# Optimization experiments

Measured on AMD Instinct MI355X. Metric: run time of the kernel, lower is better.

Reference implementation:

```python
import jax, jax.numpy as jnp
import numpy as np

B, S, I = 64, 32, 64
N_ITEMS = 100000
E, H = 256, 128


def setup_inputs() -> dict:
    key = jax.random.key(0)
    k_len, k_ids, k_ut, k_emb, k_wih, k_whh, k_a1, k_a2, k_vt = jax.random.split(key, 9)
    n_sess = B * S
    # ragged session lengths in [2, I] -> trailing zero padding, all sessions valid
    lengths = jax.random.randint(k_len, (n_sess,), 2, I + 1)
    ids = jax.random.randint(k_ids, (n_sess, I), 1, N_ITEMS + 1)
    pad_mask = jnp.arange(I)[None, :] < lengths[:, None]
    item_id = (ids * pad_mask).reshape(B, S, I).astype(jnp.int32)
    eval_from = jnp.zeros((B,), dtype=jnp.int32)
    u_type = jax.random.randint(k_ut, (B,), 0, 5).astype(jnp.int32)
    sc = 0.05
    emb = jax.random.normal(k_emb, (N_ITEMS + 1, E), jnp.float32) * sc
    emb = emb.at[0].set(0.0)  # padding_idx=0
    W_ih = jax.random.normal(k_wih, (3 * H, E), jnp.float32) * sc
    W_hh = jax.random.normal(k_whh, (3 * H, H), jnp.float32) * sc
    b_ih = jnp.zeros((3 * H,), jnp.float32)
    b_hh = jnp.zeros((3 * H,), jnp.float32)
    W_a1 = jax.random.normal(k_a1, (H, H), jnp.float32) * sc
    W_a2 = jax.random.normal(k_a2, (H, H), jnp.float32) * sc
    W_vt = jax.random.normal(k_vt, (1, H), jnp.float32) * sc
    return {"item_id": item_id, "eval_from": eval_from, "u_type": u_type,
            "emb": emb, "W_ih": W_ih, "W_hh": W_hh, "b_ih": b_ih, "b_hh": b_hh,
            "W_a1": W_a1, "W_a2": W_a2, "W_vt": W_vt}


def _gru(x, lengths, W_ih, W_hh, b_ih, b_hh):
    # x: [L, N, E]; packed-GRU semantics: state frozen past each length,
    # outputs zero at padded steps (matches pad_packed_sequence).
    L, N, _ = x.shape
    Hh = W_hh.shape[1]

    def step(h, inp):
        xt, t = inp
        gi = xt @ W_ih.T + b_ih           # [N, 3H]
        gh = h @ W_hh.T + b_hh
        i_r, i_z, i_n = jnp.split(gi, 3, axis=-1)
        h_r, h_z, h_n = jnp.split(gh, 3, axis=-1)
        r = jax.nn.sigmoid(i_r + h_r)
        z = jax.nn.sigmoid(i_z + h_z)
        n = jnp.tanh(i_n + r * h_n)
        h_new = (1.0 - z) * n + z * h
        valid = (t < lengths)[:, None]
        h_next = jnp.where(valid, h_new, h)
        out = jnp.where(valid, h_new, 0.0)
        return h_next, out

    h0 = jnp.zeros((N, Hh), x.dtype)
    hT, outs = jax.lax.scan(step, h0, (x, jnp.arange(L)))
    return outs, hT  # outs: [L, N, H], hT: [N, H]


def reference(item_id, eval_from, u_type, emb, W_ih, W_hh, b_ih, b_hh, W_a1, W_a2, W_vt):
    b, s, i = item_id.shape
    ids = jnp.clip(item_id, 0)
    allow = jnp.arange(s)[None, :] >= eval_from[:, None]        # [B, S]
    ids = ids * allow[:, :, None].astype(ids.dtype)
    sess = ids.reshape(b * s, i)                                # [N, I]
    lengths = (sess != 0).sum(1)                                # all >= 2 by construction
    n = sess.shape[0]
    target = sess[jnp.arange(n), lengths - 1]
    len_in = lengths - 1
    L = i - 1  # static L_in_max; extra padded steps are masked out
    mask = (jnp.arange(L)[None, :] < len_in[:, None])           # [N, L]
    inp = sess[:, :L] * mask.astype(sess.dtype)
    x = emb[inp]                                                # [N, L, E] (dropout=identity, eval)
    outs, ht = _gru(x.transpose(1, 0, 2), len_in, W_ih, W_hh, b_ih, b_hh)
    gru = outs.transpose(1, 0, 2)                               # [N, L, H]
    q1 = jnp.einsum('nlh,kh->nlk', gru, W_a1)
    q2 = (ht @ W_a2.T)[:, None, :]
    alpha = jnp.einsum('nlh,oh->nlo', jax.nn.sigmoid(q1 + q2), W_vt)[..., 0] * mask
    c_loc = jnp.einsum('nl,nlh->nh', alpha, gru)
    reps = jnp.concatenate([c_loc, ht], axis=1)                 # [N, 2H] (ct dropout=identity)
    u = jnp.repeat(u_type, s)
    return reps, target, u
```

## Files before the change

### kernel.cpp

```cpp
#include <hip/hip_runtime.h>
#include <hip/hip_bf16.h>

#define NSESS 2048
#define NI 64
#define LL 63
#define EE 256
#define HH 128
#define GG 384

typedef __attribute__((ext_vector_type(8))) short short8;
typedef __attribute__((ext_vector_type(4))) float f32x4;

static __device__ __forceinline__ unsigned short f2b(float f) {
  union { float f; unsigned u; } v; v.f = f;
  unsigned r = (v.u + 0x7FFFu + ((v.u >> 16) & 1u)) >> 16;
  return (unsigned short)r;
}
static __device__ __forceinline__ float b2f(unsigned short s) {
  union { unsigned u; float f; } v; v.u = ((unsigned)s) << 16;
  return v.f;
}
static __device__ __forceinline__ float lo16(unsigned u) {
  union { unsigned v; float f; } x; x.v = u << 16; return x.f;
}
static __device__ __forceinline__ float hi16(unsigned u) {
  union { unsigned v; float f; } x; x.v = u & 0xFFFF0000u; return x.f;
}
static __device__ __forceinline__ float sigmoidf_(float x) {
  return 1.f / (1.f + __expf(-x));
}
static __device__ __forceinline__ float tanh2_(float y) {
  float e = __expf(2.f * y);
  return 1.f - 2.f / (1.f + e);
}
static __device__ __forceinline__ void barrier_lds_only() {
  asm volatile("s_waitcnt lgkmcnt(0)" ::: "memory");
  __builtin_amdgcn_sched_barrier(0);
  __builtin_amdgcn_s_barrier();
  __builtin_amdgcn_sched_barrier(0);
}

__global__ __launch_bounds__(64) void prep_kernel(const int* __restrict__ item_id,
                                                  const int* __restrict__ eval_from,
                                                  const int* __restrict__ u_type,
                                                  int* __restrict__ len_in,
                                                  int* __restrict__ inp,
                                                  float* __restrict__ out) {
  int n = blockIdx.x;
  int lane = threadIdx.x;
  int b = n >> 5, s = n & 31;
  int allow = (s >= eval_from[b]) ? 1 : 0;
  int id = item_id[n * NI + lane];
  if (id < 0) id = 0;
  id *= allow;
  unsigned long long m = __ballot(id != 0);
  int length = __popcll(m);
  int li = length - 1;
  int tv = __shfl(id, (length > 0) ? (length - 1) : 0, 64);
  int target = (length > 0) ? tv : 0;
  if (lane < LL) inp[n * LL + lane] = (lane < li) ? id : 0;
  if (lane == 0) {
    len_in[n] = li;
    out[NSESS * 256 + n] = (float)target;
    out[NSESS * 256 + NSESS + n] = (float)u_type[b];
  }
}

__global__ __launch_bounds__(256) void cvt_weights(const float* __restrict__ W_ih,
                                                   const float* __restrict__ W_hh,
                                                   const float* __restrict__ W_a1,
                                                   unsigned short* __restrict__ Wb,
                                                   unsigned short* __restrict__ Whs,
                                                   unsigned short* __restrict__ Wa1b) {
  int i = blockIdx.x * 256 + threadIdx.x;
  Wb[i] = f2b(W_ih[i]);
  if (i < GG * HH) Whs[i] = f2b(W_hh[i]);
  if (i < HH * HH) Wa1b[i] = f2b(W_a1[i]);
}

__global__ __launch_bounds__(512, 2) void gemm_in(const float* __restrict__ emb,
                                                  const unsigned short* __restrict__ Wb,
                                                  const float* __restrict__ b_ih,
                                                  const int* __restrict__ inp,
                                                  unsigned short* __restrict__ gi) {
  constexpr int XP = 264;
  __shared__ unsigned short Ash[2][16 * XP];

  const int t = threadIdx.x;
  const int lane = t & 63, w = t >> 6;
  const int ccol = lane & 15, kg = lane >> 4;
  const int g0 = w * 48;

  short8 bfr[3][8];
#pragma unroll
  for (int nt = 0; nt < 3; ++nt) {
    const unsigned short* wrow = Wb + (long)(g0 + nt * 16 + ccol) * EE + kg * 8;
#pragma unroll
    for (int c = 0; c < 8; ++c) bfr[nt][c] = *(const short8*)(wrow + c * 32);
  }
  float bias[3];
#pragma unroll
  for (int nt = 0; nt < 3; ++nt) bias[nt] = b_ih[g0 + nt * 16 + ccol];

  const int tile0 = blockIdx.x * 8;
  const int srow = t >> 5;
  const int scol = (t & 31) * 8;

  {
    long rid = inp[tile0 * 16 + srow];
    const float* x = emb + rid * EE + scol;
    float4 a0 = *(const float4*)x, a1 = *(const float4*)(x + 4);
    short8 v;
    v[0]=(short)f2b(a0.x); v[1]=(short)f2b(a0.y); v[2]=(short)f2b(a0.z); v[3]=(short)f2b(a0.w);
    v[4]=(short)f2b(a1.x); v[5]=(short)f2b(a1.y); v[6]=(short)f2b(a1.z); v[7]=(short)f2b(a1.w);
    *(short8*)(&Ash[0][srow * XP + scol]) = v;
  }
  __syncthreads();

  for (int i = 0; i < 8; ++i) {
    const int cur = i & 1;
    const int m0 = (tile0 + i) * 16;

    float4 a0, a1;
    if (i + 1 < 8) {
      long rid = inp[(tile0 + i + 1) * 16 + srow];
      const float* x = emb + rid * EE + scol;
      a0 = *(const float4*)x; a1 = *(const float4*)(x + 4);
    }

    f32x4 acc[3];
#pragma unroll
    for (int nt = 0; nt < 3; ++nt)
      acc[nt] = (f32x4){bias[nt], bias[nt], bias[nt], bias[nt]};
#pragma unroll
    for (int c = 0; c < 8; ++c) {
      short8 af = *(const short8*)(&Ash[cur][ccol * XP + c * 32 + kg * 8]);
#pragma unroll
      for (int nt = 0; nt < 3; ++nt)
        acc[nt] = __builtin_amdgcn_mfma_f32_16x16x32_bf16(af, bfr[nt][c], acc[nt], 0, 0, 0);
    }

    long base[4];
#pragma unroll
    for (int j = 0; j < 4; ++j) {
      int m = m0 + kg * 4 + j;
      int n = m / 63;
      int l = m - 63 * n;
      base[j] = ((long)l * NSESS + n) * GG;
    }
#pragma unroll
    for (int nt = 0; nt < 3; ++nt) {
      int g = g0 + nt * 16 + ccol;
#pragma unroll
      for (int j = 0; j < 4; ++j)
        gi[base[j] + g] = f2b(acc[nt][j]);
    }

    if (i + 1 < 8) {
      short8 v;
      v[0]=(short)f2b(a0.x); v[1]=(short)f2b(a0.y); v[2]=(short)f2b(a0.z); v[3]=(short)f2b(a0.w);
      v[4]=(short)f2b(a1.x); v[5]=(short)f2b(a1.y); v[6]=(short)f2b(a1.z); v[7]=(short)f2b(a1.w);
      *(short8*)(&Ash[cur ^ 1][srow * XP + scol]) = v;
    }
    barrier_lds_only();
  }
}

__global__ __launch_bounds__(512) void gru_mfma(const unsigned short* __restrict__ Whs,
                                                const float* __restrict__ b_hh,
                                                const unsigned short* __restrict__ gi,
                                                const int* __restrict__ len_in,
                                                unsigned short* __restrict__ outs,
                                                float* __restrict__ ht,
                                                float* __restrict__ out) {
  __shared__ unsigned short ring[2 * 2048];

  const int t = threadIdx.x;
  const int w = t >> 6, lane = t & 63;
  const int ccol = lane & 15, kg = lane >> 4;
  const int n0 = blockIdx.x * 16;
  const int jh = w * 16 + ccol;
  const int p0 = w * 16 + kg * 4;
  const int swz = (ccol & 7) << 3;

  short8 bfr[3][4];
#pragma unroll
  for (int cls = 0; cls < 3; ++cls) {
    const unsigned short* wrow = Whs + (long)(cls * HH + jh) * HH;
#pragma unroll
    for (int c = 0; c < 4; ++c)
      bfr[cls][c] = *(const short8*)(wrow + c * 32 + kg * 8);
  }
  f32x4 bhv[3];
#pragma unroll
  for (int cls = 0; cls < 3; ++cls)
    bhv[cls] = *(const f32x4*)(b_hh + cls * HH + p0);

  const int li = len_in[n0 + ccol];
  float hold[4] = {0.f, 0.f, 0.f, 0.f};

  for (int idx = t; idx < 2 * 2048; idx += 512) ring[idx] = 0;

  const unsigned short* gbase = gi + (long)(n0 + ccol) * GG + p0;
  const long lstride = (long)NSESS * GG;
#define GA(l, cls) ((const uint2*)(gbase + (long)(l) * lstride + (cls) * HH))

  uint2 gA[3], gB[3];
#pragma unroll
  for (int cls = 0; cls < 3; ++cls) gA[cls] = *GA(0, cls);
#pragma unroll
  for (int cls = 0; cls < 3; ++cls) gB[cls] = *GA(1, cls);

  barrier_lds_only();

  auto step = [&](int l, uint2 (&gbuf)[3]) {
    float gvv[3][4];
#pragma unroll
    for (int cls = 0; cls < 3; ++cls) {
      gvv[cls][0] = lo16(gbuf[cls].x); gvv[cls][1] = hi16(gbuf[cls].x);
      gvv[cls][2] = lo16(gbuf[cls].y); gvv[cls][3] = hi16(gbuf[cls].y);
    }
    if (l + 2 < LL) {
#pragma unroll
      for (int cls = 0; cls < 3; ++cls) gbuf[cls] = *GA(l + 2, cls);
    }

    const unsigned short* rb = ring + ((l + 1) & 1) * 2048 + ccol * HH;
    short8 hf[4];
#pragma unroll
    for (int c = 0; c < 4; ++c)
      hf[c] = *(const short8*)(rb + ((c * 32 + kg * 8) ^ swz));

    f32x4 acc[3];
#pragma unroll
    for (int cls = 0; cls < 3; ++cls) {
      acc[cls] = bhv[cls];
#pragma unroll
      for (int c = 0; c < 4; ++c)
        acc[cls] = __builtin_amdgcn_mfma_f32_16x16x32_bf16(bfr[cls][c], hf[c], acc[cls], 0, 0, 0);
    }

    bool valid = (l < li);
#pragma unroll
    for (int j = 0; j < 4; ++j) {
      float rg = sigmoidf_(gvv[0][j] + acc[0][j]);
      float zg = sigmoidf_(gvv[1][j] + acc[1][j]);
      float ng = tanh2_(gvv[2][j] + rg * acc[2][j]);
      float hnew = ng + zg * (hold[j] - ng);
      hold[j] = valid ? hnew : hold[j];
    }
    uint2 hp;
    hp.x = (unsigned)f2b(hold[0]) | ((unsigned)f2b(hold[1]) << 16);
    hp.y = (unsigned)f2b(hold[2]) | ((unsigned)f2b(hold[3]) << 16);
    *(uint2*)(ring + (l & 1) * 2048 + ccol * HH + (((w * 16 + kg * 4)) ^ swz)) = hp;
    uint2 ov = valid ? hp : (uint2){0u, 0u};
    *(uint2*)(outs + ((long)(n0 + ccol) * LL + l) * HH + p0) = ov;
    barrier_lds_only();
  };

  for (int b2 = 0; b2 < 31; ++b2) {
    step(2 * b2, gA);
    step(2 * b2 + 1, gB);
  }
  step(62, gA);
#undef GA

  f32x4 hv = {hold[0], hold[1], hold[2], hold[3]};
  *(f32x4*)(ht + (long)(n0 + ccol) * HH + p0) = hv;
  *(f32x4*)(out + (long)(n0 + ccol) * 256 + HH + p0) = hv;
}

__global__ __launch_bounds__(256) void attn(const unsigned short* __restrict__ outs,
                                            const float* __restrict__ ht,
                                            const unsigned short* __restrict__ Wa1b,
                                            const float* __restrict__ W_a2,
                                            const float* __restrict__ W_vt,
                                            const int* __restrict__ len_in,
                                            float* __restrict__ out) {
  constexpr int OP = HH + 8;
  __shared__ unsigned short o_l[64 * OP];
  __shared__ float q2s[HH];
  __shared__ float wvt[HH];
  __shared__ float hts[HH];
  __shared__ float aw[4][64];
  __shared__ float alphas[64];

  const int n = blockIdx.x;
  const int t = threadIdx.x;
  const int lane = t & 63, wv = t >> 6;
  const int ccol = lane & 15, kg = lane >> 4;
  const int li = len_in[n];

  const unsigned* src = (const unsigned*)(outs + (long)n * LL * HH);
  for (int idx = t; idx < LL * 64; idx += 256) {
    int r = idx >> 6, c2 = idx & 63;
    ((unsigned*)(o_l + r * OP))[c2] = src[r * 64 + c2];
  }
  if (t < 64) ((unsigned*)(o_l + 63 * OP))[t] = 0;
  if (t < HH) { hts[t] = ht[(long)n * HH + t]; wvt[t] = W_vt[t]; }

  short8 bfr[2][4];
#pragma unroll
  for (int nt = 0; nt < 2; ++nt) {
    int G = wv * 32 + nt * 16 + ccol;
#pragma unroll
    for (int c = 0; c < 4; ++c)
      bfr[nt][c] = *(const short8*)(Wa1b + (long)G * HH + c * 32 + kg * 8);
  }
  __syncthreads();

  if (t < HH) {
    float a = 0.f;
    const float* w2 = W_a2 + t * HH;
    for (int k = 0; k < HH; ++k) a += hts[k] * w2[k];
    q2s[t] = a;
  }
  __syncthreads();

  f32x4 acc[4][2];
#pragma unroll
  for (int mt = 0; mt < 4; ++mt)
#pragma unroll
    for (int nt = 0; nt < 2; ++nt) acc[mt][nt] = (f32x4){0.f, 0.f, 0.f, 0.f};
#pragma unroll
  for (int mt = 0; mt < 4; ++mt) {
#pragma unroll
    for (int c = 0; c < 4; ++c) {
      short8 af = *(const short8*)(o_l + (mt * 16 + ccol) * OP + c * 32 + kg * 8);
#pragma unroll
      for (int nt = 0; nt < 2; ++nt)
        acc[mt][nt] = __builtin_amdgcn_mfma_f32_16x16x32_bf16(af, bfr[nt][c], acc[mt][nt], 0, 0, 0);
    }
  }

  float q2v[2], wvv[2];
#pragma unroll
  for (int nt = 0; nt < 2; ++nt) {
    int cg = wv * 32 + nt * 16 + ccol;
    q2v[nt] = q2s[cg]; wvv[nt] = wvt[cg];
  }
#pragma unroll
  for (int mt = 0; mt < 4; ++mt) {
    float part[4] = {0.f, 0.f, 0.f, 0.f};
#pragma unroll
    for (int nt = 0; nt < 2; ++nt)
#pragma unroll
      for (int j = 0; j < 4; ++j)
        part[j] += sigmoidf_(acc[mt][nt][j] + q2v[nt]) * wvv[nt];
#pragma unroll
    for (int j = 0; j < 4; ++j) {
#pragma unroll
      for (int off = 1; off < 16; off <<= 1)
        part[j] += __shfl_xor(part[j], off, 64);
    }
    if (ccol == 0) {
#pragma unroll
      for (int j = 0; j < 4; ++j) aw[wv][mt * 16 + kg * 4 + j] = part[j];
    }
  }
  __syncthreads();

  if (t < 64) {
    float s = aw[0][t] + aw[1][t] + aw[2][t] + aw[3][t];
    alphas[t] = (t < li) ? s : 0.f;
  }
  __syncthreads();

  if (t < HH) {
    float c = 0.f;
    for (int l = 0; l < LL; ++l) c = fmaf(alphas[l], b2f(o_l[l * OP + t]), c);
    out[(long)n * 256 + t] = c;
  }
}

extern "C" void kernel_launch(void* const* d_in, const int* in_sizes, int n_in,
                              void* d_out, int out_size, void* d_ws, size_t ws_size,
                              hipStream_t stream) {
  (void)in_sizes; (void)n_in; (void)out_size; (void)ws_size;
  const int* item_id   = (const int*)d_in[0];
  const int* eval_from = (const int*)d_in[1];
  const int* u_type    = (const int*)d_in[2];
  const float* emb     = (const float*)d_in[3];
  const float* W_ih    = (const float*)d_in[4];
  const float* W_hh    = (const float*)d_in[5];
  const float* b_ih    = (const float*)d_in[6];
  const float* b_hh    = (const float*)d_in[7];
  const float* W_a1    = (const float*)d_in[8];
  const float* W_a2    = (const float*)d_in[9];
  const float* W_vt    = (const float*)d_in[10];

  float* out = (float*)d_out;
  char* ws = (char*)d_ws;
  int* len_in           = (int*)(ws + 0);
  int* inp              = (int*)(ws + 8192);
  unsigned short* Wb    = (unsigned short*)(ws + 524288);
  unsigned short* Whs   = (unsigned short*)(ws + 720896);
  float* ht             = (float*)(ws + 819200);
  unsigned short* gi    = (unsigned short*)(ws + 1867776);
  unsigned short* outs  = (unsigned short*)(ws + 100958208);
  unsigned short* Wa1b  = (unsigned short*)(ws + 133988352);

  prep_kernel<<<NSESS, 64, 0, stream>>>(item_id, eval_from, u_type, len_in, inp, out);
  cvt_weights<<<384, 256, 0, stream>>>(W_ih, W_hh, W_a1, Wb, Whs, Wa1b);
  gemm_in<<<1008, 512, 0, stream>>>(emb, Wb, b_ih, inp, gi);
  gru_mfma<<<NSESS / 16, 512, 0, stream>>>(Whs, b_hh, gi, len_in, outs, ht, out);
  attn<<<NSESS, 512, 0, stream>>>(outs, ht, Wa1b, W_a2, W_vt, len_in, out);
}
```

Baseline: 139.8 us.

## Load embedding fragments directly into registers in gemm_in, drop LDS staging

The input-projection GEMM no longer stages embedding rows in double-buffered shared memory behind barriers. Each wave now gathers its own A fragments straight from global memory, converts them to bf16 in registers and feeds the MFMAs. Blocks shrink to 4 waves and the grid doubles, with each wave owning one 48-column slice of the gate outputs. This removes LDS traffic and barriers, but each embedding row is now read by eight waves instead of once per block, which leans heavily on cache reuse, and the loads are no longer prefetched a tile ahead. The attention launch is also reduced to 256 threads to match its launch bounds.

```diff
diff --git a/kernel.cpp b/kernel.cpp
--- a/kernel.cpp
+++ b/kernel.cpp
@@ -78,18 +78,17 @@
   if (i < HH * HH) Wa1b[i] = f2b(W_a1[i]);
 }
 
-__global__ __launch_bounds__(512, 2) void gemm_in(const float* __restrict__ emb,
+__global__ __launch_bounds__(256, 2) void gemm_in(const float* __restrict__ emb,
                                                   const unsigned short* __restrict__ Wb,
                                                   const float* __restrict__ b_ih,
                                                   const int* __restrict__ inp,
                                                   unsigned short* __restrict__ gi) {
-  constexpr int XP = 264;
-  __shared__ unsigned short Ash[2][16 * XP];
-
   const int t = threadIdx.x;
   const int lane = t & 63, w = t >> 6;
   const int ccol = lane & 15, kg = lane >> 4;
-  const int g0 = w * 48;
+  const long J = (long)blockIdx.x * 4 + w;
+  const int g0 = (int)(J & 7) * 48;
+  const int mbase = (int)(J >> 3) * 8;
 
   short8 bfr[3][8];
 #pragma unroll
@@ -102,39 +101,30 @@
 #pragma unroll
   for (int nt = 0; nt < 3; ++nt) bias[nt] = b_ih[g0 + nt * 16 + ccol];
 
-  const int tile0 = blockIdx.x * 8;
-  const int srow = t >> 5;
-  const int scol = (t & 31) * 8;
-
-  {
-    long rid = inp[tile0 * 16 + srow];
-    const float* x = emb + rid * EE + scol;
-    float4 a0 = *(const float4*)x, a1 = *(const float4*)(x + 4);
-    short8 v;
-    v[0]=(short)f2b(a0.x); v[1]=(short)f2b(a0.y); v[2]=(short)f2b(a0.z); v[3]=(short)f2b(a0.w);
-    v[4]=(short)f2b(a1.x); v[5]=(short)f2b(a1.y); v[6]=(short)f2b(a1.z); v[7]=(short)f2b(a1.w);
-    *(short8*)(&Ash[0][srow * XP + scol]) = v;
-  }
-  __syncthreads();
-
   for (int i = 0; i < 8; ++i) {
-    const int cur = i & 1;
-    const int m0 = (tile0 + i) * 16;
-
-    float4 a0, a1;
-    if (i + 1 < 8) {
-      long rid = inp[(tile0 + i + 1) * 16 + srow];
-      const float* x = emb + rid * EE + scol;
-      a0 = *(const float4*)x; a1 = *(const float4*)(x + 4);
+    const int m = mbase + i;
+    long rid = inp[m * 16 + ccol];
+    const float* xrow = emb + rid * EE + kg * 8;
+
+    float4 L[16];
+#pragma unroll
+    for (int c = 0; c < 8; ++c) {
+      L[2 * c]     = *(const float4*)(xrow + c * 32);
+      L[2 * c + 1] = *(const float4*)(xrow + c * 32 + 4);
     }
 
     f32x4 acc[3];
 #pragma unroll
     for (int nt = 0; nt < 3; ++nt)
       acc[nt] = (f32x4){bias[nt], bias[nt], bias[nt], bias[nt]};
+
 #pragma unroll
     for (int c = 0; c < 8; ++c) {
-      short8 af = *(const short8*)(&Ash[cur][ccol * XP + c * 32 + kg * 8]);
+      short8 af;
+      af[0] = (short)f2b(L[2 * c].x);     af[1] = (short)f2b(L[2 * c].y);
+      af[2] = (short)f2b(L[2 * c].z);     af[3] = (short)f2b(L[2 * c].w);
+      af[4] = (short)f2b(L[2 * c + 1].x); af[5] = (short)f2b(L[2 * c + 1].y);
+      af[6] = (short)f2b(L[2 * c + 1].z); af[7] = (short)f2b(L[2 * c + 1].w);
 #pragma unroll
       for (int nt = 0; nt < 3; ++nt)
         acc[nt] = __builtin_amdgcn_mfma_f32_16x16x32_bf16(af, bfr[nt][c], acc[nt], 0, 0, 0);
@@ -143,9 +133,9 @@
     long base[4];
 #pragma unroll
     for (int j = 0; j < 4; ++j) {
-      int m = m0 + kg * 4 + j;
-      int n = m / 63;
-      int l = m - 63 * n;
+      int mrow = m * 16 + kg * 4 + j;
+      int n = mrow / 63;
+      int l = mrow - 63 * n;
       base[j] = ((long)l * NSESS + n) * GG;
     }
 #pragma unroll
@@ -155,14 +145,6 @@
       for (int j = 0; j < 4; ++j)
         gi[base[j] + g] = f2b(acc[nt][j]);
     }
-
-    if (i + 1 < 8) {
-      short8 v;
-      v[0]=(short)f2b(a0.x); v[1]=(short)f2b(a0.y); v[2]=(short)f2b(a0.z); v[3]=(short)f2b(a0.w);
-      v[4]=(short)f2b(a1.x); v[5]=(short)f2b(a1.y); v[6]=(short)f2b(a1.z); v[7]=(short)f2b(a1.w);
-      *(short8*)(&Ash[cur ^ 1][srow * XP + scol]) = v;
-    }
-    barrier_lds_only();
   }
 }
 
@@ -252,7 +234,7 @@
     uint2 hp;
     hp.x = (unsigned)f2b(hold[0]) | ((unsigned)f2b(hold[1]) << 16);
     hp.y = (unsigned)f2b(hold[2]) | ((unsigned)f2b(hold[3]) << 16);
-    *(uint2*)(ring + (l & 1) * 2048 + ccol * HH + (((w * 16 + kg * 4)) ^ swz)) = hp;
+    *(uint2*)(ring + (l & 1) * 2048 + ccol * HH + (p0 ^ swz)) = hp;
     uint2 ov = valid ? hp : (uint2){0u, 0u};
     *(uint2*)(outs + ((long)(n0 + ccol) * LL + l) * HH + p0) = ov;
     barrier_lds_only();
@@ -402,7 +384,7 @@
 
   prep_kernel<<<NSESS, 64, 0, stream>>>(item_id, eval_from, u_type, len_in, inp, out);
   cvt_weights<<<384, 256, 0, stream>>>(W_ih, W_hh, W_a1, Wb, Whs, Wa1b);
-  gemm_in<<<1008, 512, 0, stream>>>(emb, Wb, b_ih, inp, gi);
+  gemm_in<<<2016, 256, 0, stream>>>(emb, Wb, b_ih, inp, gi);
   gru_mfma<<<NSESS / 16, 512, 0, stream>>>(Whs, b_hh, gi, len_in, outs, ht, out);
-  attn<<<NSESS, 512, 0, stream>>>(outs, ht, Wa1b, W_a2, W_vt, len_in, out);
-}
+  attn<<<NSESS, 256, 0, stream>>>(outs, ht, Wa1b, W_a2, W_vt, len_in, out);
+}
```

New measurement: 245.4 us. +75.5%, slower.
